# Kernel tuning notes

Measured on AMD Instinct MI355X. Metric: run time of the kernel, lower is better.

Reference implementation:

```python
import jax, jax.numpy as jnp
import numpy as np

DM = 512; NH = 8; EL = 3; FACTOR = 3; EPS = 1e-5

def layernorm(x, g, b):
    m = x.mean(-1, keepdims=True)
    v = x.var(-1, keepdims=True)
    return (x - m) / jnp.sqrt(v + EPS) * g + b

def pos_embed(L, d):
    pos = jnp.arange(L, dtype=jnp.float32)[:, None]
    div = jnp.exp(jnp.arange(0, d, 2, dtype=jnp.float32) * (-np.log(10000.0) / d))
    pe = jnp.zeros((L, d), jnp.float32)
    pe = pe.at[:, 0::2].set(jnp.sin(pos * div))
    pe = pe.at[:, 1::2].set(jnp.cos(pos * div))
    return pe

def circ_conv1d(x, w, b=None):
    # x: [B,L,Cin], w: [Cout,Cin,3]; torch Conv1d padding=1, padding_mode='circular'
    xp = jnp.concatenate([x[:, -1:], x, x[:, :1]], axis=1)
    y = jax.lax.conv_general_dilated(xp, w, (1,), 'VALID', dimension_numbers=('NWC', 'OIW', 'NWC'))
    return y if b is None else y + b

def prob_attention(q, k, v, rng):
    # q,k,v: [B,H,L,D] -- Informer ProbSparse attention (non-masked encoder case)
    B, H, L, D = q.shape
    LK = k.shape[2]
    U = min(int(FACTOR * np.ceil(np.log(LK))), LK)   # sampled keys per query
    u = min(int(FACTOR * np.ceil(np.log(L))), L)     # top queries kept
    idx = jax.random.randint(rng, (L, U), 0, LK)     # shared across B,H as in torch
    k_samp = k[:, :, idx]                            # [B,H,L,U,D]
    qk = jnp.einsum('bhld,bhlud->bhlu', q, k_samp)
    M = qk.max(-1) - qk.sum(-1) / LK                 # sparsity measure
    top = jax.lax.top_k(M, u)[1]                     # [B,H,u]
    q_red = jnp.take_along_axis(q, top[..., None], axis=2)
    scores = jnp.einsum('bhud,bhkd->bhuk', q_red, k) / jnp.sqrt(jnp.asarray(D, q.dtype))
    attn = jax.nn.softmax(scores, axis=-1)
    upd = jnp.einsum('bhuk,bhkd->bhud', attn, v)
    ctx = jnp.broadcast_to(v.mean(axis=2, keepdims=True), (B, H, L, D))
    bi = jnp.arange(B)[:, None, None]
    hi = jnp.arange(H)[None, :, None]
    return ctx.at[bi, hi, top].set(upd)

def encoder_layer(x, p, rng):
    Wq_, bq_, Wk_, bk_, Wv_, bv_, Wo_, bo_, w1, b1, w2, b2, g1, be1, g2, be2 = p
    B, L, _ = x.shape
    D = DM // NH
    q = (x @ Wq_.T + bq_).reshape(B, L, NH, D).transpose(0, 2, 1, 3)
    k = (x @ Wk_.T + bk_).reshape(B, L, NH, D).transpose(0, 2, 1, 3)
    v = (x @ Wv_.T + bv_).reshape(B, L, NH, D).transpose(0, 2, 1, 3)
    ctx = prob_attention(q, k, v, rng).transpose(0, 2, 1, 3).reshape(B, L, DM)
    x = x + (ctx @ Wo_.T + bo_)
    x = layernorm(x, g1, be1)
    y = jax.nn.gelu(x @ w1.T + b1, approximate=False)  # pointwise conv1 (k=1)
    y = y @ w2.T + b2                                   # pointwise conv2 (k=1)
    return layernorm(x + y, g2, be2)

def distil_layer(x, w, b, g, beta):
    y = circ_conv1d(x, w, b)                 # Conv1d k=3 circular
    mu = y.mean((0, 1))
    var = y.var((0, 1))                      # BatchNorm1d, training stats
    y = (y - mu) / jnp.sqrt(var + EPS) * g + beta
    y = jax.nn.elu(y)
    # MaxPool1d(kernel=3, stride=2, padding=1)
    return jax.lax.reduce_window(y, -jnp.inf, jax.lax.max, (1, 3, 1), (1, 2, 1), ((0, 0), (1, 1), (0, 0)))

def setup_inputs():
    key = jax.random.key(0)
    ks = jax.random.split(key, 12)
    B, S, CIN, COUT, DFF = 8, 2048, 7, 7, 2048
    r = lambda k, s: jax.random.normal(k, s, jnp.float32)
    return {
        'x_enc': r(ks[0], (B, S, CIN)),
        'tok_w': r(ks[1], (DM, CIN, 3)) * (2.0 / (CIN * 3)) ** 0.5,
        'Wq': r(ks[2], (EL, DM, DM)) * DM ** -0.5, 'bq': jnp.zeros((EL, DM)),
        'Wk': r(ks[3], (EL, DM, DM)) * DM ** -0.5, 'bk': jnp.zeros((EL, DM)),
        'Wv': r(ks[4], (EL, DM, DM)) * DM ** -0.5, 'bv': jnp.zeros((EL, DM)),
        'Wo': r(ks[5], (EL, DM, DM)) * DM ** -0.5, 'bo': jnp.zeros((EL, DM)),
        'conv1_w': r(ks[6], (EL, DFF, DM)) * DM ** -0.5, 'conv1_b': jnp.zeros((EL, DFF)),
        'conv2_w': r(ks[7], (EL, DM, DFF)) * DFF ** -0.5, 'conv2_b': jnp.zeros((EL, DM)),
        'ln1_g': jnp.ones((EL, DM)), 'ln1_b': jnp.zeros((EL, DM)),
        'ln2_g': jnp.ones((EL, DM)), 'ln2_b': jnp.zeros((EL, DM)),
        'dconv_w': r(ks[8], (EL - 1, DM, DM, 3)) * (DM * 3) ** -0.5, 'dconv_b': jnp.zeros((EL - 1, DM)),
        'bn_g': jnp.ones((EL - 1, DM)), 'bn_b': jnp.zeros((EL - 1, DM)),
        'lnf_g': jnp.ones((DM,)), 'lnf_b': jnp.zeros((DM,)),
        'end_w': r(ks[9], (COUT, DM)) * DM ** -0.5, 'end_b': jnp.zeros((COUT,)),
    }

def reference(x_enc, tok_w, Wq, bq, Wk, bk, Wv, bv, Wo, bo, conv1_w, conv1_b, conv2_w, conv2_b, ln1_g, ln1_b, ln2_g, ln2_b, dconv_w, dconv_b, bn_g, bn_b, lnf_g, lnf_b, end_w, end_b):
    x = circ_conv1d(x_enc, tok_w) + pos_embed(x_enc.shape[1], DM)  # DataEmbedding
    base = jax.random.key(42)
    for l in range(EL):
        p = (Wq[l], bq[l], Wk[l], bk[l], Wv[l], bv[l], Wo[l], bo[l],
             conv1_w[l], conv1_b[l], conv2_w[l], conv2_b[l],
             ln1_g[l], ln1_b[l], ln2_g[l], ln2_b[l])
        x = encoder_layer(x, p, jax.random.fold_in(base, l))
        if l < EL - 1:
            x = distil_layer(x, dconv_w[l], dconv_b[l], bn_g[l], bn_b[l])
    x = layernorm(x, lnf_g, lnf_b)
    return x @ end_w.T + end_b  # end_conv2 (Conv1d k=1)
```

## Files before the change

### kernel.cpp

```cpp
#include <hip/hip_runtime.h>
#include <cstdint>
#include <cstddef>

#define DMODEL 512
#define NHEAD 8
#define HD 64

typedef float f32x4 __attribute__((ext_vector_type(4)));
typedef _Float16 f16x8 __attribute__((ext_vector_type(8)));
typedef _Float16 f16x4 __attribute__((ext_vector_type(4)));

__device__ __forceinline__ uint32_t rotl32(uint32_t x, int r) {
  return (x << r) | (x >> (32 - r));
}

__device__ __forceinline__ void tf_block(uint32_t k0, uint32_t k1,
                                         uint32_t& x0, uint32_t& x1) {
  uint32_t ks0 = k0, ks1 = k1, ks2 = k0 ^ k1 ^ 0x1BD11BDAu;
  x0 += ks0; x1 += ks1;
  x0 += x1; x1 = rotl32(x1, 13); x1 ^= x0;
  x0 += x1; x1 = rotl32(x1, 15); x1 ^= x0;
  x0 += x1; x1 = rotl32(x1, 26); x1 ^= x0;
  x0 += x1; x1 = rotl32(x1, 6);  x1 ^= x0;
  x0 += ks1; x1 += ks2 + 1u;
  x0 += x1; x1 = rotl32(x1, 17); x1 ^= x0;
  x0 += x1; x1 = rotl32(x1, 29); x1 ^= x0;
  x0 += x1; x1 = rotl32(x1, 16); x1 ^= x0;
  x0 += x1; x1 = rotl32(x1, 24); x1 ^= x0;
  x0 += ks2; x1 += ks0 + 2u;
  x0 += x1; x1 = rotl32(x1, 13); x1 ^= x0;
  x0 += x1; x1 = rotl32(x1, 15); x1 ^= x0;
  x0 += x1; x1 = rotl32(x1, 26); x1 ^= x0;
  x0 += x1; x1 = rotl32(x1, 6);  x1 ^= x0;
  x0 += ks0; x1 += ks1 + 3u;
  x0 += x1; x1 = rotl32(x1, 17); x1 ^= x0;
  x0 += x1; x1 = rotl32(x1, 29); x1 ^= x0;
  x0 += x1; x1 = rotl32(x1, 16); x1 ^= x0;
  x0 += x1; x1 = rotl32(x1, 24); x1 ^= x0;
  x0 += ks1; x1 += ks2 + 4u;
  x0 += x1; x1 = rotl32(x1, 13); x1 ^= x0;
  x0 += x1; x1 = rotl32(x1, 15); x1 ^= x0;
  x0 += x1; x1 = rotl32(x1, 26); x1 ^= x0;
  x0 += x1; x1 = rotl32(x1, 6);  x1 ^= x0;
  x0 += ks2; x1 += ks0 + 5u;
}

__global__ void idx_kernel(int* __restrict__ idxb, int n, int layer, int mask) {
  int e = blockIdx.x * 256 + threadIdx.x;
  if (e >= n) return;
  uint32_t f0 = 0u, f1 = (uint32_t)layer;
  tf_block(0u, 42u, f0, f1);
  uint32_t s0 = 0u, s1 = 1u;
  tf_block(f0, f1, s0, s1);
  uint32_t x0 = 0u, x1 = (uint32_t)e;
  tf_block(s0, s1, x0, x1);
  uint32_t bits = x0 ^ x1;
  idxb[e] = (int)(bits & (uint32_t)mask);
}

__device__ __forceinline__ float gelu_f(float v) {
  return 0.5f * v * (1.0f + erff(v * 0.7071067811865476f));
}

template <int ACT, int HASR, int CONV, int PART>
__global__ __launch_bounds__(256, 2) void gemm128(
    const float* __restrict__ A, const void* __restrict__ Wsp,
    const float* __restrict__ bias, const float* Rres, float* C,
    int N, int K, int Lmask, int ntx, int nty, int kloop, int ks) {
  __shared__ __align__(16) _Float16 sm[2][4][128][32];
  const _Float16* Wh = (const _Float16*)Wsp;
  const _Float16* Wl = Wh + (size_t)N * K;
  const int tid = threadIdx.x;
  int blk = blockIdx.x;
  const int tiles = ntx * nty;
  int kb = 0;
  if (PART) { kb = blk / tiles; blk -= kb * tiles; }
  const int koff = kb * kloop;
  const int xcd = blk & 7;
  const int j = blk >> 3;
  const int jr = j / ntx;
  const int row_t = xcd * (nty >> 3) + jr;
  const int col_t = j - jr * ntx;
  const int row0 = row_t * 128, col0 = col_t * 128;

  const int r4 = tid >> 2;
  const int ss = tid & 3;

  const float* Ap0 = A + (size_t)(row0 + r4) * K + koff + ss * 8;
  const float* Ap1 = A + (size_t)(row0 + 64 + r4) * K + koff + ss * 8;
  const _Float16* Wh0 = Wh + (size_t)(col0 + r4) * K + koff + ss * 8;
  const _Float16* Wh1 = Wh + (size_t)(col0 + 64 + r4) * K + koff + ss * 8;
  const _Float16* Wl0 = Wl + (size_t)(col0 + r4) * K + koff + ss * 8;
  const _Float16* Wl1 = Wl + (size_t)(col0 + 64 + r4) * K + koff + ss * 8;
  int tcv0 = 0, bb0 = 0, tcv1 = 0, bb1 = 0;
  if (CONV) {
    int a0 = row0 + r4, a1 = row0 + 64 + r4;
    tcv0 = a0 & Lmask; bb0 = a0 & ~Lmask;
    tcv1 = a1 & Lmask; bb1 = a1 & ~Lmask;
  }

  const int lane = tid & 63;
  const int wv = tid >> 6;
  const int wr = (wv >> 1) << 6;
  const int wc = (wv & 1) << 6;
  const int fr = lane & 15;
  const int fs = lane >> 4;

  f32x4 acc[4][4];
  {
    f32x4 z = {0.f, 0.f, 0.f, 0.f};
#pragma unroll
    for (int r = 0; r < 4; ++r)
#pragma unroll
      for (int c = 0; c < 4; ++c) acc[r][c] = z;
  }

  f32x4 ra[4], rwh[2], rwl[2];
  f16x8 wfh[4], wfl[4], afh[4], afl[4];

  auto gload = [&](int k0) {
    const float *a0p, *a1p;
    if (CONV) {
      int kabs = koff + k0 + ss * 8;
      int w = kabs >> 9, cq = kabs & 511;
      a0p = A + (size_t)(bb0 | ((tcv0 - 1 + w) & Lmask)) * 512 + cq;
      a1p = A + (size_t)(bb1 | ((tcv1 - 1 + w) & Lmask)) * 512 + cq;
    } else {
      a0p = Ap0 + k0;
      a1p = Ap1 + k0;
    }
    ra[0] = *(const f32x4*)(a0p);
    ra[1] = *(const f32x4*)(a0p + 4);
    ra[2] = *(const f32x4*)(a1p);
    ra[3] = *(const f32x4*)(a1p + 4);
    rwh[0] = *(const f32x4*)(Wh0 + k0);
    rwh[1] = *(const f32x4*)(Wh1 + k0);
    rwl[0] = *(const f32x4*)(Wl0 + k0);
    rwl[1] = *(const f32x4*)(Wl1 + k0);
  };

  auto stage = [&](int buf) {
#pragma unroll
    for (int p = 0; p < 2; ++p) {
      const int row = (p << 6) + r4;
      const int sl = (ss ^ ((row >> 1) & 3)) << 3;
      float tmp[8];
      *(f32x4*)(tmp) = ra[2 * p];
      *(f32x4*)(tmp + 4) = ra[2 * p + 1];
      _Float16 hv[8], lv[8];
#pragma unroll
      for (int q = 0; q < 8; ++q) {
        _Float16 h = (_Float16)tmp[q];
        hv[q] = h;
        lv[q] = (_Float16)(tmp[q] - (float)h);
      }
      *(f16x8*)&sm[buf][0][row][sl] = *(f16x8*)hv;
      *(f16x8*)&sm[buf][1][row][sl] = *(f16x8*)lv;
      *(f32x4*)&sm[buf][2][row][sl] = rwh[p];
      *(f32x4*)&sm[buf][3][row][sl] = rwl[p];
    }
  };

  auto readfrags = [&](int buf) {
#pragma unroll
    for (int c = 0; c < 4; ++c) {
      const int row = wc + (c << 4) + fr;
      const int sl = (fs ^ ((row >> 1) & 3)) << 3;
      wfh[c] = *(const f16x8*)&sm[buf][2][row][sl];
      wfl[c] = *(const f16x8*)&sm[buf][3][row][sl];
    }
#pragma unroll
    for (int r = 0; r < 4; ++r) {
      const int row = wr + (r << 4) + fr;
      const int sl = (fs ^ ((row >> 1) & 3)) << 3;
      afh[r] = *(const f16x8*)&sm[buf][0][row][sl];
      afl[r] = *(const f16x8*)&sm[buf][1][row][sl];
    }
  };

  const int T = kloop >> 5;
  int cur = 0;
  gload(0);
  stage(0);
  if (T > 1) gload(1 << 5);
  __syncthreads();
  readfrags(0);

  for (int it = 0; it < T; ++it) {
    if (it + 1 < T) stage(cur ^ 1);
    if (it + 2 < T) gload((it + 2) << 5);
    __builtin_amdgcn_s_setprio(1);
#pragma unroll
    for (int r = 0; r < 4; ++r)
#pragma unroll
      for (int c = 0; c < 4; ++c)
        acc[r][c] = __builtin_amdgcn_mfma_f32_16x16x32_f16(afh[r], wfh[c],
                                                           acc[r][c], 0, 0, 0);
#pragma unroll
    for (int r = 0; r < 4; ++r)
#pragma unroll
      for (int c = 0; c < 4; ++c)
        acc[r][c] = __builtin_amdgcn_mfma_f32_16x16x32_f16(afh[r], wfl[c],
                                                           acc[r][c], 0, 0, 0);
#pragma unroll
    for (int r = 0; r < 4; ++r)
#pragma unroll
      for (int c = 0; c < 4; ++c)
        acc[r][c] = __builtin_amdgcn_mfma_f32_16x16x32_f16(afl[r], wfh[c],
                                                           acc[r][c], 0, 0, 0);
    __builtin_amdgcn_s_setprio(0);
    if (it + 1 < T) {
      __syncthreads();
      cur ^= 1;
      readfrags(cur);
    }
  }

  const int crow = fs << 2;
  if (PART) {
    float* Cp = C + (size_t)kb * ((size_t)(nty << 7)) * N;
#pragma unroll
    for (int r = 0; r < 4; ++r) {
      const int m0 = row0 + wr + (r << 4) + crow;
#pragma unroll
      for (int c = 0; c < 4; ++c) {
        const int n0 = col0 + wc + (c << 4) + fr;
#pragma unroll
        for (int q = 0; q < 4; ++q)
          Cp[(size_t)(m0 + q) * N + n0] = acc[r][c][q];
      }
    }
  } else {
#pragma unroll
    for (int r = 0; r < 4; ++r) {
      const int m0 = row0 + wr + (r << 4) + crow;
#pragma unroll
      for (int c = 0; c < 4; ++c) {
        const int n0 = col0 + wc + (c << 4) + fr;
        const float bcol = bias[n0];
#pragma unroll
        for (int q = 0; q < 4; ++q) {
          float v = acc[r][c][q] + bcol;
          if (HASR) v += Rres[(size_t)(m0 + q) * N + n0];
          if (ACT == 1) v = gelu_f(v);
          C[(size_t)(m0 + q) * N + n0] = v;
        }
      }
    }
  }
}

template <int HASR>
__global__ __launch_bounds__(256) void combine_kernel(
    const float* __restrict__ part, const float* __restrict__ bias,
    const float* Rres, float* __restrict__ Cout, size_t MN, int ks) {
  size_t gid = (size_t)blockIdx.x * 256 + threadIdx.x;
  int c = (int)(gid & 511);
  float v = 0.f;
  for (int kb = 0; kb < ks; kb++) v += part[kb * MN + gid];
  v += bias[c];
  if (HASR) v += Rres[gid];
  Cout[gid] = v;
}

__global__ __launch_bounds__(256) void splitw_kernel(const float* __restrict__ w,
                                                     _Float16* __restrict__ o,
                                                     int n) {
  int g = (blockIdx.x * 256 + threadIdx.x) << 2;
  if (g >= n) return;
  f32x4 f = *(const f32x4*)(w + g);
  f16x4 hv, lv;
#pragma unroll
  for (int q = 0; q < 4; ++q) {
    _Float16 h = (_Float16)f[q];
    hv[q] = h;
    lv[q] = (_Float16)(f[q] - (float)h);
  }
  *(f16x4*)(o + g) = hv;
  *(f16x4*)(o + n + g) = lv;
}

__global__ void tokpe_kernel(const float* __restrict__ xe,
                             const float* __restrict__ w,
                             float* __restrict__ out, int S) {
  int gid = blockIdx.x * 256 + threadIdx.x;
  int o = gid & 511;
  int bt = gid >> 9;
  int t = bt % S, b = bt / S;
  float acc = 0.f;
#pragma unroll
  for (int ww = 0; ww < 3; ww++) {
    int tt = t - 1 + ww;
    tt = (tt < 0) ? tt + S : (tt >= S ? tt - S : tt);
    const float* xr = xe + ((size_t)(b * S + tt)) * 7;
#pragma unroll
    for (int i = 0; i < 7; i++) acc += xr[i] * w[o * 21 + i * 3 + ww];
  }
  int i2 = o >> 1;
  float dv = expf((float)(2 * i2) * (-9.210340371976184f / 512.0f));
  float ang = (float)t * dv;
  acc += (o & 1) ? cosf(ang) : sinf(ang);
  out[gid] = acc;
}

__global__ void packw_kernel(const float* __restrict__ dw,
                             _Float16* __restrict__ wp) {
  int gid = blockIdx.x * 256 + threadIdx.x;
  int o = gid / 1536;
  int kk = gid - o * 1536;
  int ww = kk / 512;
  int c = kk - ww * 512;
  float v = dw[((size_t)o * 512 + c) * 3 + ww];
  _Float16 h = (_Float16)v;
  wp[gid] = h;
  wp[786432 + gid] = (_Float16)(v - (float)h);
}

__global__ __launch_bounds__(256, 8) void mscore_kernel(
    const float* __restrict__ Q, const float* __restrict__ Kb,
    const int* __restrict__ idxb, float* __restrict__ Mout, int L, int U) {
  int i = blockIdx.x;
  int b = i & 7;
  int j = i >> 3;
  int tid = threadIdx.x;
  int qd = tid >> 2;
  int q = tid & 3;
  int h = qd & 7;
  int t = j * 8 + (qd >> 3);
  const float* qp = Q + ((size_t)(b * L + t)) * DMODEL + h * HD + q * 4;
  float4 qv0 = *(const float4*)(qp);
  float4 qv1 = *(const float4*)(qp + 16);
  float4 qv2 = *(const float4*)(qp + 32);
  float4 qv3 = *(const float4*)(qp + 48);
  const float* Kh = Kb + (size_t)b * L * DMODEL + h * HD + q * 4;
  const int* ip = idxb + t * U;
  float mx = -3.4e38f, sm = 0.f;
  int kr = ip[0];
  for (int jj = 0; jj < U; jj++) {
    const float* kp = Kh + (size_t)kr * DMODEL;
    float4 k0 = *(const float4*)(kp);
    float4 k1 = *(const float4*)(kp + 16);
    float4 k2 = *(const float4*)(kp + 32);
    float4 k3 = *(const float4*)(kp + 48);
    if (jj + 1 < U) kr = ip[jj + 1];
    float d = qv0.x * k0.x + qv0.y * k0.y + qv0.z * k0.z + qv0.w * k0.w +
              qv1.x * k1.x + qv1.y * k1.y + qv1.z * k1.z + qv1.w * k1.w +
              qv2.x * k2.x + qv2.y * k2.y + qv2.z * k2.z + qv2.w * k2.w +
              qv3.x * k3.x + qv3.y * k3.y + qv3.z * k3.z + qv3.w * k3.w;
    d += __shfl_xor(d, 1);
    d += __shfl_xor(d, 2);
    mx = fmaxf(mx, d);
    sm += d;
  }
  if (q == 0) Mout[(size_t)(b * 8 + h) * L + t] = mx - sm / (float)L;
}

__global__ __launch_bounds__(256) void topk_kernel(const float* __restrict__ Mv,
                                                   int* __restrict__ topb, int L,
                                                   int u) {
  __shared__ float wv_s[4];
  __shared__ int wi_s[4];
  __shared__ int best_s;
  int bh = blockIdx.x, tid = threadIdx.x;
  int lane = tid & 63, w = tid >> 6;
  int cnt = L >> 8;
  float lv[8];
  for (int i = 0; i < cnt; i++) lv[i] = Mv[(size_t)bh * L + i * 256 + tid];
  for (int r = 0; r < u; r++) {
    float bv = -3.4e38f;
    int bi = 0x7fffffff;
    for (int i = 0; i < cnt; i++) {
      if (lv[i] > bv) { bv = lv[i]; bi = i * 256 + tid; }
    }
    for (int s = 32; s > 0; s >>= 1) {
      float ov = __shfl_down(bv, s);
      int oi = __shfl_down(bi, s);
      if (ov > bv || (ov == bv && oi < bi)) { bv = ov; bi = oi; }
    }
    if (lane == 0) { wv_s[w] = bv; wi_s[w] = bi; }
    __syncthreads();
    if (tid == 0) {
      float fv = wv_s[0];
      int fi = wi_s[0];
      for (int q = 1; q < 4; q++) {
        if (wv_s[q] > fv || (wv_s[q] == fv && wi_s[q] < fi)) {
          fv = wv_s[q];
          fi = wi_s[q];
        }
      }
      best_s = fi;
      topb[bh * u + r] = fi;
    }
    __syncthreads();
    int win = best_s;
    if ((win & 255) == tid) lv[win >> 8] = -3.4e38f;
  }
}

__global__ void gatherq_kernel(const float* __restrict__ Q,
                               const int* __restrict__ topb,
                               float* __restrict__ qsel, int L, int u) {
  int i = blockIdx.x;
  int bh = i / u;
  int b = bh >> 3, h = bh & 7;
  int t = topb[i];
  qsel[i * HD + threadIdx.x] =
      Q[((size_t)(b * L + t)) * DMODEL + h * HD + threadIdx.x];
}

__global__ __launch_bounds__(256) void xmean_kernel(const float* __restrict__ x,
                                                    float* __restrict__ psumx,
                                                    int L) {
  int i = blockIdx.x;
  int b = i >> 3, g = i & 7;
  int rows = L >> 3;
  int tid = threadIdx.x;
  const float* base = x + ((size_t)b * L + (size_t)g * rows) * DMODEL;
  float s0 = 0.f, s1 = 0.f;
  for (int t = 0; t < rows; t++) {
    s0 += base[(size_t)t * DMODEL + tid];
    s1 += base[(size_t)t * DMODEL + tid + 256];
  }
  psumx[i * DMODEL + tid] = s0;
  psumx[i * DMODEL + tid + 256] = s1;
}

__global__ __launch_bounds__(256) void mvmake_kernel(
    const float* __restrict__ psumx, const float* __restrict__ Wv,
    const float* __restrict__ bv, const float* __restrict__ Wo,
    const float* __restrict__ bo, float* __restrict__ mvg,
    float* __restrict__ mvWog, int L) {
  __shared__ float xm[512];
  __shared__ float mvs[512];
  int b = blockIdx.x, tid = threadIdx.x;
  float inv = 1.0f / (float)L;
  for (int nn = 0; nn < 2; nn++) {
    int c = tid + nn * 256;
    float s = 0.f;
    for (int g = 0; g < 8; g++) s += psumx[(b * 8 + g) * DMODEL + c];
    xm[c] = s * inv;
  }
  __syncthreads();
  for (int nn = 0; nn < 2; nn++) {
    int n = tid + nn * 256;
    const float* wr = Wv + (size_t)n * 512;
    float s = bv[n];
    for (int k = 0; k < 512; k += 4) {
      float4 w4 = *(const float4*)(wr + k);
      s += xm[k] * w4.x + xm[k + 1] * w4.y + xm[k + 2] * w4.z + xm[k + 3] * w4.w;
    }
    mvs[n] = s;
    mvg[b * DMODEL + n] = s;
  }
  __syncthreads();
  for (int nn = 0; nn < 2; nn++) {
    int n = tid + nn * 256;
    const float* wr = Wo + (size_t)n * 512;
    float s = bo[n];
    for (int k = 0; k < 512; k += 4) {
      float4 w4 = *(const float4*)(wr + k);
      s += mvs[k] * w4.x + mvs[k + 1] * w4.y + mvs[k + 2] * w4.z +
           mvs[k + 3] * w4.w;
    }
    mvWog[b * DMODEL + n] = s;
  }
}

__global__ void x1bcast_kernel(const float* __restrict__ x,
                               const float* __restrict__ mvWog,
                               float* __restrict__ x1, int L) {
  int gid = blockIdx.x * 256 + threadIdx.x;
  int c = gid & 511;
  int r = gid >> 9;
  int b = r / L;
  x1[gid] = x[gid] + mvWog[b * DMODEL + c];
}

__global__ __launch_bounds__(256) void attnflash_kernel(
    const float* __restrict__ qsel, const float* __restrict__ Kb,
    const float* __restrict__ Vb, float* __restrict__ pm,
    float* __restrict__ pl, float* __restrict__ pO, int L, int u, int nchunk) {
  __shared__ float qs[24][64];
  __shared__ float Kt[64][68];
  __shared__ float Ps[24][68];
  int blk = blockIdx.x;
  int bh = blk / nchunk;
  int c = blk - bh * nchunk;
  int b = bh >> 3, h = bh & 7;
  int cs = L / nchunk;
  int tid = threadIdx.x;
  int lane = tid & 63;
  int w = tid >> 6;
  for (int i = tid; i < u * 64; i += 256)
    qs[i >> 6][i & 63] = qsel[(size_t)bh * u * 64 + i];
  float m[6], l[6], O[6];
#pragma unroll
  for (int k = 0; k < 6; k++) { m[k] = -3.4e38f; l[k] = 0.f; O[k] = 0.f; }
  const float* Kbase = Kb + (size_t)b * L * DMODEL + h * HD;
  const float* Vbase = Vb + (size_t)b * L * DMODEL + h * HD;
  const int jrow = tid & 63;
  const int dch = (tid >> 6) << 4;
  for (int j0 = c * cs; j0 < (c + 1) * cs; j0 += 64) {
    __syncthreads();
    const float* kr = Kbase + (size_t)(j0 + jrow) * DMODEL + dch;
    float4 k0 = *(const float4*)(kr);
    float4 k1 = *(const float4*)(kr + 4);
    float4 k2 = *(const float4*)(kr + 8);
    float4 k3 = *(const float4*)(kr + 12);
#pragma unroll
    for (int q = 0; q < 4; q++) {
      Kt[dch + q][jrow] = ((float*)&k0)[q];
      Kt[dch + 4 + q][jrow] = ((float*)&k1)[q];
      Kt[dch + 8 + q][jrow] = ((float*)&k2)[q];
      Kt[dch + 12 + q][jrow] = ((float*)&k3)[q];
    }
    __syncthreads();
#pragma unroll
    for (int k = 0; k < 6; k++) {
      int qi = 4 * k + w;
      if (qi >= u) break;
      float s = 0.f;
#pragma unroll
      for (int d = 0; d < 64; d++) s += qs[qi][d] * Kt[d][lane];
      s *= 0.125f;
      float mx = s;
#pragma unroll
      for (int off = 32; off > 0; off >>= 1)
        mx = fmaxf(mx, __shfl_down(mx, off));
      mx = __shfl(mx, 0);
      float mnew = fmaxf(m[k], mx);
      float p = expf(s - mnew);
      float ps = p;
#pragma unroll
      for (int off = 32; off > 0; off >>= 1) ps += __shfl_down(ps, off);
      ps = __shfl(ps, 0);
      float alpha = expf(m[k] - mnew);
      l[k] = l[k] * alpha + ps;
      m[k] = mnew;
      O[k] *= alpha;
      Ps[qi][lane] = p;
    }
    for (int j = 0; j < 64; j += 4) {
      float v0 = Vbase[(size_t)(j0 + j) * DMODEL + lane];
      float v1 = Vbase[(size_t)(j0 + j + 1) * DMODEL + lane];
      float v2 = Vbase[(size_t)(j0 + j + 2) * DMODEL + lane];
      float v3 = Vbase[(size_t)(j0 + j + 3) * DMODEL + lane];
#pragma unroll
      for (int k = 0; k < 6; k++) {
        int qi = 4 * k + w;
        if (qi >= u) break;
        O[k] += Ps[qi][j] * v0 + Ps[qi][j + 1] * v1 + Ps[qi][j + 2] * v2 +
                Ps[qi][j + 3] * v3;
      }
    }
  }
#pragma unroll
  for (int k = 0; k < 6; k++) {
    int qi = 4 * k + w;
    if (qi < u) {
      int p = (bh * nchunk + c) * u + qi;
      if (lane == 0) { pm[p] = m[k]; pl[p] = l[k]; }
      pO[(size_t)p * 64 + lane] = O[k];
    }
  }
}

__global__ __launch_bounds__(256) void deltaWo_kernel(
    const float* __restrict__ pm, const float* __restrict__ pl,
    const float* __restrict__ pO, const float* __restrict__ mvg,
    const int* __restrict__ topb, const float* __restrict__ Wo, float* x1,
    int L, int u, int nchunk) {
  __shared__ float ds[64];
  int sel = blockIdx.x;
  int bh = sel / u;
  int qi = sel - bh * u;
  int b = bh >> 3, h = bh & 7;
  int t = topb[sel];
  int tid = threadIdx.x;
  if (tid < 64) {
    float mstar = -3.4e38f;
    for (int c = 0; c < nchunk; c++)
      mstar = fmaxf(mstar, pm[(bh * nchunk + c) * u + qi]);
    float lstar = 0.f, O = 0.f;
    for (int c = 0; c < nchunk; c++) {
      int p = (bh * nchunk + c) * u + qi;
      float wgt = expf(pm[p] - mstar);
      lstar += wgt * pl[p];
      O += wgt * pO[(size_t)p * 64 + tid];
    }
    ds[tid] = O / lstar - mvg[b * DMODEL + h * HD + tid];
  }
  __syncthreads();
  float* row = x1 + ((size_t)(b * L + t)) * DMODEL;
  for (int nn = 0; nn < 2; nn++) {
    int n = tid + nn * 256;
    const float* wr = Wo + (size_t)n * 512 + h * HD;
    float a = 0.f;
#pragma unroll
    for (int k = 0; k < 64; k += 4) {
      float4 w4 = *(const float4*)(wr + k);
      a += ds[k] * w4.x + ds[k + 1] * w4.y + ds[k + 2] * w4.z + ds[k + 3] * w4.w;
    }
    atomicAdd(row + n, a);
  }
}

__global__ __launch_bounds__(256) void ln_kernel(const float* __restrict__ X,
                                                 const float* __restrict__ g,
                                                 const float* __restrict__ bta,
                                                 float* __restrict__ Y) {
  int row = blockIdx.x * 4 + (threadIdx.x >> 6);
  int lane = threadIdx.x & 63;
  size_t base = (size_t)row * DMODEL + lane * 8;
  float4 a = *(const float4*)(X + base);
  float4 b = *(const float4*)(X + base + 4);
  float s = a.x + a.y + a.z + a.w + b.x + b.y + b.z + b.w;
#pragma unroll
  for (int off = 32; off > 0; off >>= 1) s += __shfl_xor(s, off);
  float mean = s * (1.0f / 512.0f);
  float d[8];
  d[0] = a.x - mean; d[1] = a.y - mean; d[2] = a.z - mean; d[3] = a.w - mean;
  d[4] = b.x - mean; d[5] = b.y - mean; d[6] = b.z - mean; d[7] = b.w - mean;
  float q = 0.f;
#pragma unroll
  for (int i = 0; i < 8; ++i) q += d[i] * d[i];
#pragma unroll
  for (int off = 32; off > 0; off >>= 1) q += __shfl_xor(q, off);
  float inv = 1.0f / sqrtf(q * (1.0f / 512.0f) + 1e-5f);
  int col = lane * 8;
  float4 g0 = *(const float4*)(g + col);
  float4 g1 = *(const float4*)(g + col + 4);
  float4 t0 = *(const float4*)(bta + col);
  float4 t1 = *(const float4*)(bta + col + 4);
  float4 y0, y1;
  y0.x = d[0] * inv * g0.x + t0.x; y0.y = d[1] * inv * g0.y + t0.y;
  y0.z = d[2] * inv * g0.z + t0.z; y0.w = d[3] * inv * g0.w + t0.w;
  y1.x = d[4] * inv * g1.x + t1.x; y1.y = d[5] * inv * g1.y + t1.y;
  y1.z = d[6] * inv * g1.z + t1.z; y1.w = d[7] * inv * g1.w + t1.w;
  *(float4*)(Y + base) = y0;
  *(float4*)(Y + base + 4) = y1;
}

__global__ __launch_bounds__(256) void bnpart_kernel(const float* __restrict__ z,
                                                     float* __restrict__ psum,
                                                     float* __restrict__ psq,
                                                     int rowsPer) {
  int blk = blockIdx.x, tid = threadIdx.x;
  size_t r0 = (size_t)blk * rowsPer;
  float s0 = 0, q0 = 0, s1 = 0, q1 = 0;
  for (int r = 0; r < rowsPer; r++) {
    const float* zp = z + (r0 + r) * DMODEL;
    float a = zp[tid];
    s0 += a; q0 += a * a;
    float c = zp[tid + 256];
    s1 += c; q1 += c * c;
  }
  psum[blk * DMODEL + tid] = s0;
  psum[blk * DMODEL + tid + 256] = s1;
  psq[blk * DMODEL + tid] = q0;
  psq[blk * DMODEL + tid + 256] = q1;
}

__global__ void bnfin_kernel(const float* __restrict__ psum,
                             const float* __restrict__ psq, float* __restrict__ mu,
                             float* __restrict__ var, int nb, int Rtot) {
  int c = blockIdx.x * 256 + threadIdx.x;
  float s = 0, q = 0;
  for (int b = 0; b < nb; b++) {
    s += psum[b * DMODEL + c];
    q += psq[b * DMODEL + c];
  }
  float m = s / (float)Rtot;
  mu[c] = m;
  var[c] = fmaxf(q / (float)Rtot - m * m, 0.f);
}

__global__ void bnpool_kernel(const float* __restrict__ z,
                              const float* __restrict__ mu,
                              const float* __restrict__ var,
                              const float* __restrict__ g,
                              const float* __restrict__ bta,
                              float* __restrict__ out, int L) {
  int gid = blockIdx.x * 256 + threadIdx.x;
  int c = gid & 511;
  int bt = gid >> 9;
  int L2 = L >> 1;
  int t2 = bt % L2, b = bt / L2;
  float m = mu[c];
  float inv = 1.0f / sqrtf(var[c] + 1e-5f);
  float gg = g[c], bb = bta[c];
  float best = -3.4e38f;
#pragma unroll
  for (int ww = 0; ww < 3; ww++) {
    int t = 2 * t2 - 1 + ww;
    if (t < 0 || t >= L) continue;
    float yv = (z[((size_t)(b * L + t)) * DMODEL + c] - m) * inv * gg + bb;
    yv = (yv > 0.f) ? yv : expm1f(yv);
    best = fmaxf(best, yv);
  }
  out[gid] = best;
}

__global__ __launch_bounds__(64) void end_kernel(const float* __restrict__ xn,
                                                 const float* __restrict__ ew,
                                                 const float* __restrict__ eb,
                                                 float* __restrict__ out) {
  __shared__ float xs[512];
  __shared__ float red[64];
  int row = blockIdx.x, tid = threadIdx.x;
#pragma unroll
  for (int i = 0; i < 8; i++) xs[tid + 64 * i] = xn[(size_t)row * DMODEL + tid + 64 * i];
  __syncthreads();
  for (int c = 0; c < 7; c++) {
    float p = 0.f;
    for (int d = tid; d < 512; d += 64) p += xs[d] * ew[c * DMODEL + d];
    red[tid] = p;
    __syncthreads();
    for (int s = 32; s > 0; s >>= 1) {
      if (tid < s) red[tid] += red[tid + s];
      __syncthreads();
    }
    if (tid == 0) out[row * 7 + c] = red[0] + eb[c];
    __syncthreads();
  }
}

extern "C" void kernel_launch(void* const* d_in, const int* in_sizes, int n_in,
                              void* d_out, int out_size, void* d_ws,
                              size_t ws_size, hipStream_t stream) {
  (void)in_sizes; (void)n_in; (void)out_size;
  const float* x_enc = (const float*)d_in[0];
  const float* tok_w = (const float*)d_in[1];
  const float* Wq = (const float*)d_in[2];
  const float* bq = (const float*)d_in[3];
  const float* Wk = (const float*)d_in[4];
  const float* bk = (const float*)d_in[5];
  const float* Wv = (const float*)d_in[6];
  const float* bv = (const float*)d_in[7];
  const float* Wo = (const float*)d_in[8];
  const float* bo = (const float*)d_in[9];
  const float* w1 = (const float*)d_in[10];
  const float* b1 = (const float*)d_in[11];
  const float* w2 = (const float*)d_in[12];
  const float* b2 = (const float*)d_in[13];
  const float* g1 = (const float*)d_in[14];
  const float* be1 = (const float*)d_in[15];
  const float* g2 = (const float*)d_in[16];
  const float* be2 = (const float*)d_in[17];
  const float* dw = (const float*)d_in[18];
  const float* db = (const float*)d_in[19];
  const float* bng = (const float*)d_in[20];
  const float* bnb = (const float*)d_in[21];
  const float* lnfg = (const float*)d_in[22];
  const float* lnfb = (const float*)d_in[23];
  const float* endw = (const float*)d_in[24];
  const float* endb = (const float*)d_in[25];
  float* out = (float*)d_out;
  char* ws = (char*)d_ws;

  const int NCHMAX = 32;

  size_t o = 0;
  float* buf0 = (float*)(ws + o); o += (size_t)16384 * 512 * 4;
  float* qbuf = (float*)(ws + o); o += (size_t)16384 * 512 * 4;
  float* kbuf = (float*)(ws + o); o += (size_t)16384 * 512 * 4;
  float* wpack = (float*)(ws + o); o += (size_t)512 * 1536 * 4;
  float* Mb    = (float*)(ws + o); o += (size_t)64 * 2048 * 4;
  int*   idxb  = (int*)(ws + o);   o += (size_t)2048 * 24 * 4;
  int*   topb  = (int*)(ws + o);   o += 8192;
  float* qsel  = (float*)(ws + o); o += (size_t)64 * 24 * 64 * 4;
  float* mvg   = (float*)(ws + o); o += (size_t)8 * 512 * 4;
  float* mvWog = (float*)(ws + o); o += (size_t)8 * 512 * 4;
  float* psumx = (float*)(ws + o); o += (size_t)64 * 512 * 4;
  float* psum  = (float*)(ws + o); o += (size_t)128 * 512 * 4;
  float* psq   = (float*)(ws + o); o += (size_t)128 * 512 * 4;
  float* muv   = (float*)(ws + o); o += 2048;
  float* varv  = (float*)(ws + o); o += 2048;
  float* pmb   = (float*)(ws + o); o += (size_t)64 * NCHMAX * 24 * 4;
  float* plb   = (float*)(ws + o); o += (size_t)64 * NCHMAX * 24 * 4;
  float* pOb   = (float*)(ws + o); o += (size_t)64 * NCHMAX * 24 * 64 * 4;
  _Float16* wqs = (_Float16*)(ws + o); o += (size_t)512 * 512 * 4;
  _Float16* w1s = (_Float16*)(ws + o); o += (size_t)2048 * 512 * 4;
  _Float16* w2s = (_Float16*)(ws + o); o += (size_t)512 * 2048 * 4;
  float* partb = (float*)(ws + o); o += (size_t)4 * 4096 * 2048;
  const bool uks = (ws_size >= o);

  const int B = 8;
  const int S = 2048;
  tokpe_kernel<<<B * S * DMODEL / 256, 256, 0, stream>>>(x_enc, tok_w, buf0, S);

  int L = S;
  const int Uarr[3] = {24, 21, 21};
  for (int l = 0; l < 3; l++) {
    int U = Uarr[l];
    int u = Uarr[l];
    int BL = B * L;
    int nty = BL / 128;
    size_t MN = (size_t)BL * 512;
    int gq = 4 * nty;
    int ksq = (gq >= 512 || !uks) ? 1 : (512 / gq);
    int nch = L >> 6;
    idx_kernel<<<(L * U + 255) / 256, 256, 0, stream>>>(idxb, L * U, l, L - 1);

    splitw_kernel<<<256, 256, 0, stream>>>(Wq + (size_t)l * 262144, wqs, 262144);
    if (ksq == 1) {
      gemm128<0, 0, 0, 0><<<gq, 256, 0, stream>>>(
          buf0, wqs, bq + l * 512, nullptr, qbuf, 512, 512, 0, 4, nty, 512, 1);
    } else {
      gemm128<0, 0, 0, 1><<<gq * ksq, 256, 0, stream>>>(
          buf0, wqs, nullptr, nullptr, partb, 512, 512, 0, 4, nty, 512 / ksq,
          ksq);
      combine_kernel<0><<<(unsigned)(MN / 256), 256, 0, stream>>>(
          partb, bq + l * 512, nullptr, qbuf, MN, ksq);
    }
    splitw_kernel<<<256, 256, 0, stream>>>(Wk + (size_t)l * 262144, wqs, 262144);
    if (ksq == 1) {
      gemm128<0, 0, 0, 0><<<gq, 256, 0, stream>>>(
          buf0, wqs, bk + l * 512, nullptr, kbuf, 512, 512, 0, 4, nty, 512, 1);
    } else {
      gemm128<0, 0, 0, 1><<<gq * ksq, 256, 0, stream>>>(
          buf0, wqs, nullptr, nullptr, partb, 512, 512, 0, 4, nty, 512 / ksq,
          ksq);
      combine_kernel<0><<<(unsigned)(MN / 256), 256, 0, stream>>>(
          partb, bk + l * 512, nullptr, kbuf, MN, ksq);
    }
    mscore_kernel<<<L, 256, 0, stream>>>(qbuf, kbuf, idxb, Mb, L, U);
    topk_kernel<<<64, 256, 0, stream>>>(Mb, topb, L, u);
    gatherq_kernel<<<64 * u, 64, 0, stream>>>(qbuf, topb, qsel, L, u);
    xmean_kernel<<<64, 256, 0, stream>>>(buf0, psumx, L);
    mvmake_kernel<<<8, 256, 0, stream>>>(psumx, Wv + (size_t)l * 262144,
                                         bv + l * 512, Wo + (size_t)l * 262144,
                                         bo + l * 512, mvg, mvWog, L);
    splitw_kernel<<<256, 256, 0, stream>>>(Wv + (size_t)l * 262144, wqs, 262144);
    if (ksq == 1) {
      gemm128<0, 0, 0, 0><<<gq, 256, 0, stream>>>(
          buf0, wqs, bv + l * 512, nullptr, qbuf, 512, 512, 0, 4, nty, 512, 1);
    } else {
      gemm128<0, 0, 0, 1><<<gq * ksq, 256, 0, stream>>>(
          buf0, wqs, nullptr, nullptr, partb, 512, 512, 0, 4, nty, 512 / ksq,
          ksq);
      combine_kernel<0><<<(unsigned)(MN / 256), 256, 0, stream>>>(
          partb, bv + l * 512, nullptr, qbuf, MN, ksq);
    }
    attnflash_kernel<<<64 * nch, 256, 0, stream>>>(qsel, kbuf, qbuf, pmb, plb,
                                                   pOb, L, u, nch);
    x1bcast_kernel<<<(unsigned)(MN / 256), 256, 0, stream>>>(buf0, mvWog, kbuf, L);
    deltaWo_kernel<<<64 * u, 256, 0, stream>>>(pmb, plb, pOb, mvg, topb,
                                               Wo + (size_t)l * 262144, kbuf, L,
                                               u, nch);
    ln_kernel<<<BL / 4, 256, 0, stream>>>(kbuf, g1 + l * 512, be1 + l * 512, qbuf);
    splitw_kernel<<<1024, 256, 0, stream>>>(w1 + (size_t)l * 1048576, w1s,
                                            1048576);
    splitw_kernel<<<1024, 256, 0, stream>>>(w2 + (size_t)l * 1048576, w2s,
                                            1048576);
    for (int r0 = 0; r0 < BL; r0 += 4096) {
      gemm128<1, 0, 0, 0><<<16 * 32, 256, 0, stream>>>(
          qbuf + (size_t)r0 * 512, w1s, b1 + l * 2048, nullptr, buf0, 2048, 512,
          0, 16, 32, 512, 1);
      if (uks) {
        gemm128<0, 0, 0, 1><<<4 * 32 * 4, 256, 0, stream>>>(
            buf0, w2s, nullptr, nullptr, partb, 512, 2048, 0, 4, 32, 512, 4);
        combine_kernel<1><<<4096 * 512 / 256, 256, 0, stream>>>(
            partb, b2 + l * 512, qbuf + (size_t)r0 * 512,
            kbuf + (size_t)r0 * 512, (size_t)4096 * 512, 4);
      } else {
        gemm128<0, 1, 0, 0><<<4 * 32, 256, 0, stream>>>(
            buf0, w2s, b2 + l * 512, qbuf + (size_t)r0 * 512,
            kbuf + (size_t)r0 * 512, 512, 2048, 0, 4, 32, 2048, 1);
      }
    }
    ln_kernel<<<BL / 4, 256, 0, stream>>>(kbuf, g2 + l * 512, be2 + l * 512, buf0);

    if (l < 2) {
      packw_kernel<<<512 * 1536 / 256, 256, 0, stream>>>(
          dw + (size_t)l * 512 * 512 * 3, (_Float16*)wpack);
      int ksc = (gq >= 512 || !uks) ? 1 : 2;
      if (ksc == 1) {
        gemm128<0, 0, 1, 0><<<gq, 256, 0, stream>>>(
            buf0, wpack, db + l * 512, nullptr, kbuf, 512, 1536, L - 1, 4, nty,
            1536, 1);
      } else {
        gemm128<0, 0, 1, 1><<<gq * 2, 256, 0, stream>>>(
            buf0, wpack, nullptr, nullptr, partb, 512, 1536, L - 1, 4, nty, 768,
            2);
        combine_kernel<0><<<(unsigned)(MN / 256), 256, 0, stream>>>(
            partb, db + l * 512, nullptr, kbuf, MN, 2);
      }
      int nb = BL / 128;
      bnpart_kernel<<<nb, 256, 0, stream>>>(kbuf, psum, psq, 128);
      bnfin_kernel<<<2, 256, 0, stream>>>(psum, psq, muv, varv, nb, BL);
      bnpool_kernel<<<(BL / 2) * 512 / 256, 256, 0, stream>>>(
          kbuf, muv, varv, bng + l * 512, bnb + l * 512, buf0, L);
      L >>= 1;
    }
  }
  int BL = B * L;
  ln_kernel<<<BL / 4, 256, 0, stream>>>(buf0, lnfg, lnfb, qbuf);
  end_kernel<<<BL, 64, 0, stream>>>(qbuf, endw, endb, out);
}
```

Before: 2.000 ms.

## Stage GEMM tiles via direct global-to-LDS loads, split A to fp16 at fragment read

The 128x128 split-fp16 GEMM now fills shared memory with global_load_lds 16-byte transfers instead of loading through registers. A is stored in LDS as fp32 and split into hi/lo fp16 halves when each fragment is read. This removes register staging and the separate stage pass, cutting VGPR pressure and instruction count in the main loop. In exchange, A takes twice the LDS bytes, the fp32-to-fp16 split now runs once per wave instead of once per tile, and a barrier follows every iteration. There is also no explicit vmcnt wait before the barrier for the async LDS loads, which risks a race.

```diff
diff --git a/kernel.cpp b/kernel.cpp
--- a/kernel.cpp
+++ b/kernel.cpp
@@ -9,6 +9,12 @@
 typedef float f32x4 __attribute__((ext_vector_type(4)));
 typedef _Float16 f16x8 __attribute__((ext_vector_type(8)));
 typedef _Float16 f16x4 __attribute__((ext_vector_type(4)));
+
+__device__ __forceinline__ void gload16(const void* g, void* l) {
+  __builtin_amdgcn_global_load_lds(
+      (const __attribute__((address_space(1))) void*)g,
+      (__attribute__((address_space(3))) void*)l, 16, 0, 0);
+}
 
 __device__ __forceinline__ uint32_t rotl32(uint32_t x, int r) {
   return (x << r) | (x >> (32 - r));
@@ -67,7 +73,7 @@
     const float* __restrict__ A, const void* __restrict__ Wsp,
     const float* __restrict__ bias, const float* Rres, float* C,
     int N, int K, int Lmask, int ntx, int nty, int kloop, int ks) {
-  __shared__ __align__(16) _Float16 sm[2][4][128][32];
+  __shared__ __align__(16) char sm[2][32768];
   const _Float16* Wh = (const _Float16*)Wsp;
   const _Float16* Wl = Wh + (size_t)N * K;
   const int tid = threadIdx.x;
@@ -83,22 +89,6 @@
   const int col_t = j - jr * ntx;
   const int row0 = row_t * 128, col0 = col_t * 128;
 
-  const int r4 = tid >> 2;
-  const int ss = tid & 3;
-
-  const float* Ap0 = A + (size_t)(row0 + r4) * K + koff + ss * 8;
-  const float* Ap1 = A + (size_t)(row0 + 64 + r4) * K + koff + ss * 8;
-  const _Float16* Wh0 = Wh + (size_t)(col0 + r4) * K + koff + ss * 8;
-  const _Float16* Wh1 = Wh + (size_t)(col0 + 64 + r4) * K + koff + ss * 8;
-  const _Float16* Wl0 = Wl + (size_t)(col0 + r4) * K + koff + ss * 8;
-  const _Float16* Wl1 = Wl + (size_t)(col0 + 64 + r4) * K + koff + ss * 8;
-  int tcv0 = 0, bb0 = 0, tcv1 = 0, bb1 = 0;
-  if (CONV) {
-    int a0 = row0 + r4, a1 = row0 + 64 + r4;
-    tcv0 = a0 & Lmask; bb0 = a0 & ~Lmask;
-    tcv1 = a1 & Lmask; bb1 = a1 & ~Lmask;
-  }
-
   const int lane = tid & 63;
   const int wv = tid >> 6;
   const int wr = (wv >> 1) << 6;
@@ -106,6 +96,31 @@
   const int fr = lane & 15;
   const int fs = lane >> 4;
 
+  const int lsA = (lane & 7) ^ ((lane >> 3) & 7);
+  const int lsW = (lane & 3) ^ ((lane >> 3) & 3);
+
+  const float* apA[4];
+  int tcvA[4], bbA[4];
+#pragma unroll
+  for (int q = 0; q < 4; ++q) {
+    int rowc = (wv * 4 + q) * 8 + (lane >> 3);
+    int ar = row0 + rowc;
+    if (CONV) {
+      tcvA[q] = ar & Lmask;
+      bbA[q] = ar & ~Lmask;
+      apA[q] = nullptr;
+    } else {
+      apA[q] = A + (size_t)ar * K + koff + lsA * 4;
+    }
+  }
+  const _Float16 *apWh[2], *apWl[2];
+#pragma unroll
+  for (int q = 0; q < 2; ++q) {
+    int rowc = (wv * 2 + q) * 16 + (lane >> 2);
+    apWh[q] = Wh + (size_t)(col0 + rowc) * K + koff + lsW * 8;
+    apWl[q] = Wl + (size_t)(col0 + rowc) * K + koff + lsW * 8;
+  }
+
   f32x4 acc[4][4];
   {
     f32x4 z = {0.f, 0.f, 0.f, 0.f};
@@ -115,80 +130,66 @@
       for (int c = 0; c < 4; ++c) acc[r][c] = z;
   }
 
-  f32x4 ra[4], rwh[2], rwl[2];
-  f16x8 wfh[4], wfl[4], afh[4], afl[4];
-
-  auto gload = [&](int k0) {
-    const float *a0p, *a1p;
-    if (CONV) {
-      int kabs = koff + k0 + ss * 8;
-      int w = kabs >> 9, cq = kabs & 511;
-      a0p = A + (size_t)(bb0 | ((tcv0 - 1 + w) & Lmask)) * 512 + cq;
-      a1p = A + (size_t)(bb1 | ((tcv1 - 1 + w) & Lmask)) * 512 + cq;
-    } else {
-      a0p = Ap0 + k0;
-      a1p = Ap1 + k0;
-    }
-    ra[0] = *(const f32x4*)(a0p);
-    ra[1] = *(const f32x4*)(a0p + 4);
-    ra[2] = *(const f32x4*)(a1p);
-    ra[3] = *(const f32x4*)(a1p + 4);
-    rwh[0] = *(const f32x4*)(Wh0 + k0);
-    rwh[1] = *(const f32x4*)(Wh1 + k0);
-    rwl[0] = *(const f32x4*)(Wl0 + k0);
-    rwl[1] = *(const f32x4*)(Wl1 + k0);
+  f16x8 afh[4], afl[4], wfh[4], wfl[4];
+
+  auto issue = [&](int buf, int k0) {
+    char* base = sm[buf];
+#pragma unroll
+    for (int q = 0; q < 4; ++q) {
+      const float* g;
+      if (CONV) {
+        int kabs = koff + k0;
+        int w = kabs >> 9, cq = kabs & 511;
+        g = A + (size_t)(bbA[q] | ((tcvA[q] - 1 + w) & Lmask)) * 512 + cq +
+            lsA * 4;
+      } else {
+        g = apA[q] + k0;
+      }
+      gload16(g, base + (wv * 4 + q) * 1024);
+    }
+#pragma unroll
+    for (int q = 0; q < 2; ++q) {
+      gload16(apWh[q] + k0, base + 16384 + (wv * 2 + q) * 1024);
+      gload16(apWl[q] + k0, base + 24576 + (wv * 2 + q) * 1024);
+    }
   };
 
-  auto stage = [&](int buf) {
-#pragma unroll
-    for (int p = 0; p < 2; ++p) {
-      const int row = (p << 6) + r4;
-      const int sl = (ss ^ ((row >> 1) & 3)) << 3;
-      float tmp[8];
-      *(f32x4*)(tmp) = ra[2 * p];
-      *(f32x4*)(tmp + 4) = ra[2 * p + 1];
+  auto readfrags = [&](int buf) {
+    const char* base = sm[buf];
+#pragma unroll
+    for (int r = 0; r < 4; ++r) {
+      const int row = wr + (r << 4) + fr;
+      const int ps0 = (fs << 1) ^ (row & 7);
+      float t[8];
+      *(f32x4*)(t) = *(const f32x4*)(base + row * 128 + ps0 * 16);
+      *(f32x4*)(t + 4) = *(const f32x4*)(base + row * 128 + (ps0 ^ 1) * 16);
       _Float16 hv[8], lv[8];
 #pragma unroll
       for (int q = 0; q < 8; ++q) {
-        _Float16 h = (_Float16)tmp[q];
+        _Float16 h = (_Float16)t[q];
         hv[q] = h;
-        lv[q] = (_Float16)(tmp[q] - (float)h);
+        lv[q] = (_Float16)(t[q] - (float)h);
       }
-      *(f16x8*)&sm[buf][0][row][sl] = *(f16x8*)hv;
-      *(f16x8*)&sm[buf][1][row][sl] = *(f16x8*)lv;
-      *(f32x4*)&sm[buf][2][row][sl] = rwh[p];
-      *(f32x4*)&sm[buf][3][row][sl] = rwl[p];
-    }
-  };
-
-  auto readfrags = [&](int buf) {
+      afh[r] = *(f16x8*)hv;
+      afl[r] = *(f16x8*)lv;
+    }
 #pragma unroll
     for (int c = 0; c < 4; ++c) {
       const int row = wc + (c << 4) + fr;
-      const int sl = (fs ^ ((row >> 1) & 3)) << 3;
-      wfh[c] = *(const f16x8*)&sm[buf][2][row][sl];
-      wfl[c] = *(const f16x8*)&sm[buf][3][row][sl];
-    }
-#pragma unroll
-    for (int r = 0; r < 4; ++r) {
-      const int row = wr + (r << 4) + fr;
-      const int sl = (fs ^ ((row >> 1) & 3)) << 3;
-      afh[r] = *(const f16x8*)&sm[buf][0][row][sl];
-      afl[r] = *(const f16x8*)&sm[buf][1][row][sl];
+      const int ps = fs ^ ((row >> 1) & 3);
+      wfh[c] = *(const f16x8*)(base + 16384 + row * 64 + ps * 16);
+      wfl[c] = *(const f16x8*)(base + 24576 + row * 64 + ps * 16);
     }
   };
 
   const int T = kloop >> 5;
+  issue(0, 0);
+  __syncthreads();
   int cur = 0;
-  gload(0);
-  stage(0);
-  if (T > 1) gload(1 << 5);
-  __syncthreads();
-  readfrags(0);
 
   for (int it = 0; it < T; ++it) {
-    if (it + 1 < T) stage(cur ^ 1);
-    if (it + 2 < T) gload((it + 2) << 5);
+    if (it + 1 < T) issue(cur ^ 1, (it + 1) << 5);
+    readfrags(cur);
     __builtin_amdgcn_s_setprio(1);
 #pragma unroll
     for (int r = 0; r < 4; ++r)
@@ -209,11 +210,8 @@
         acc[r][c] = __builtin_amdgcn_mfma_f32_16x16x32_f16(afl[r], wfh[c],
                                                            acc[r][c], 0, 0, 0);
     __builtin_amdgcn_s_setprio(0);
-    if (it + 1 < T) {
-      __syncthreads();
-      cur ^= 1;
-      readfrags(cur);
-    }
+    __syncthreads();
+    cur ^= 1;
   }
 
   const int crow = fs << 2;
@@ -795,7 +793,7 @@
     int U = Uarr[l];
     int u = Uarr[l];
     int BL = B * L;
-    int nty = BL / 128;
+    int nty = BL >> 7;
     size_t MN = (size_t)BL * 512;
     int gq = 4 * nty;
     int ksq = (gq >= 512 || !uks) ? 1 : (512 / gq);
```

Result: no change. 1.990 ms (-0.5%).
